# Optimization experiments

Hardware: AMD Instinct MI355X
Metric: run time of the kernel (lower is better)

Reference implementation:

```python
import jax, jax.numpy as jnp
import numpy as np

N_NODES = 100000
N_EDGES = 1600000
D_IN = 128
D_OUT = 128


def setup_inputs() -> dict:
    key = jax.random.key(0)
    k1, k2, k3, k4, k5 = jax.random.split(key, 5)
    x = jax.random.normal(k1, (N_NODES, D_IN), dtype=jnp.float32)
    row = jax.random.randint(k2, (N_EDGES,), 0, N_NODES, dtype=jnp.int32)
    col = jax.random.randint(k3, (N_EDGES,), 0, N_NODES, dtype=jnp.int32)
    edge_weight = jax.random.uniform(k4, (N_EDGES,), dtype=jnp.float32)
    stdv = 1.0 / np.sqrt(D_OUT)
    weight = jax.random.uniform(k5, (D_IN, D_OUT), dtype=jnp.float32,
                                minval=-stdv, maxval=stdv)
    return {"x": x, "row": row, "col": col,
            "edge_weight": edge_weight, "weight": weight}


def reference(x, row, col, edge_weight, weight):
    # support = x @ W  -- dense feature transform [N, D_OUT]
    support = jnp.matmul(x, weight)
    # out = adj @ support, adj sparse COO: out[row] += w * support[col]
    messages = edge_weight[:, None] * support[col]  # [E, D_OUT]
    out = jax.ops.segment_sum(messages, row, num_segments=N_NODES)
    return out
```

## Files before the change

### kernel.cpp

```cpp
#include <hip/hip_runtime.h>

#define N_NODES 100000
#define N_EDGES 1600000
#define D 128
#define D4 32

#define BM 128
#define GEMM_BLOCKS ((N_NODES + BM - 1) / BM)
#define LDK 136

typedef __attribute__((ext_vector_type(8))) short short8;
typedef __attribute__((ext_vector_type(4))) float floatx4;

__device__ __forceinline__ unsigned short f2bf(float f) {
    unsigned int b = __float_as_uint(f);
    b += 0x7FFFu + ((b >> 16) & 1u);
    return (unsigned short)(b >> 16);
}
__device__ __forceinline__ float bf2f(unsigned short u) {
    return __uint_as_float((unsigned int)u << 16);
}

__global__ __launch_bounds__(256) void w_prep(
    const float* __restrict__ W, unsigned short* __restrict__ wt)
{
    int idx = blockIdx.x * 256 + threadIdx.x;
    int k = idx >> 7, n = idx & 127;
    wt[(size_t)n * D + k] = f2bf(W[idx]);
}

__global__ __launch_bounds__(256, 4) void gemm_build(
    const float* __restrict__ x, const unsigned short* __restrict__ wt,
    unsigned short* __restrict__ sup,
    const int* __restrict__ row, const int* __restrict__ col,
    const float* __restrict__ ew,
    int* __restrict__ head, int4* __restrict__ entries)
{
    __shared__ unsigned short xs[BM * LDK];

    const int tid = threadIdx.x;
    const int brow = blockIdx.x * BM;

    {
        const float4* xv = reinterpret_cast<const float4*>(x);
        #pragma unroll
        for (int i = 0; i < 16; ++i) {
            int idx = tid + i * 256;
            int r = idx >> 5, k4 = idx & 31;
            int gr = brow + r;
            float4 v = (gr < N_NODES) ? xv[(size_t)gr * D4 + k4]
                                      : make_float4(0.f, 0.f, 0.f, 0.f);
            ushort4 p;
            p.x = f2bf(v.x); p.y = f2bf(v.y); p.z = f2bf(v.z); p.w = f2bf(v.w);
            *reinterpret_cast<ushort4*>(&xs[r * LDK + k4 * 4]) = p;
        }
    }
    __syncthreads();

    const int wave = tid >> 6;
    const int lane = tid & 63;
    const int l15  = lane & 15;
    const int lkg  = lane >> 4;
    const int lk8  = lkg * 8;

    floatx4 acc[2][8];
    #pragma unroll
    for (int m = 0; m < 2; ++m)
        #pragma unroll
        for (int n = 0; n < 8; ++n) acc[m][n] = (floatx4){0.f, 0.f, 0.f, 0.f};

    const short8* bv = reinterpret_cast<const short8*>(wt);
    const int wrow = wave * 32;
    #pragma unroll
    for (int kk = 0; kk < 4; ++kk) {
        int kb = kk * 32 + lk8;
        short8 a0 = *reinterpret_cast<const short8*>(&xs[(wrow + l15) * LDK + kb]);
        short8 a1 = *reinterpret_cast<const short8*>(&xs[(wrow + 16 + l15) * LDK + kb]);
        #pragma unroll
        for (int n = 0; n < 8; ++n) {
            short8 b = bv[(n * 16 + l15) * 16 + kk * 4 + lkg];
            acc[0][n] = __builtin_amdgcn_mfma_f32_16x16x32_bf16(a0, b, acc[0][n], 0, 0, 0);
            acc[1][n] = __builtin_amdgcn_mfma_f32_16x16x32_bf16(a1, b, acc[1][n], 0, 0, 0);
        }
    }

    const int rbase = brow + wrow + lkg * 4;
    #pragma unroll
    for (int m = 0; m < 2; ++m) {
        #pragma unroll
        for (int r = 0; r < 4; ++r) {
            int grow = rbase + m * 16 + r;
            if (grow < N_NODES) {
                #pragma unroll
                for (int n = 0; n < 8; ++n)
                    sup[(size_t)grow * D + n * 16 + l15] = f2bf(acc[m][n][r]);
            }
        }
    }

    for (int e = blockIdx.x * 256 + tid; e < N_EDGES; e += GEMM_BLOCKS * 256) {
        int nx = atomicExch(&head[row[e]], e);
        entries[e] = make_int4(nx, col[e], __float_as_int(ew[e]), 0);
    }
}

__global__ __launch_bounds__(256) void gather_list(
    const int* __restrict__ head, const int4* __restrict__ entries,
    const unsigned short* __restrict__ sup, float* __restrict__ out)
{
    const int half = threadIdx.x >> 5;
    const int lane = threadIdx.x & 31;
    const int node = blockIdx.x * 8 + half;

    float4 acc = {0.f, 0.f, 0.f, 0.f};

    int e = head[node];
    while (e >= 0) {
        int4 en = entries[e];
        float w = __int_as_float(en.z);
        ushort4 s = reinterpret_cast<const ushort4*>(sup + (size_t)en.y * D)[lane];
        acc.x = fmaf(w, bf2f(s.x), acc.x);
        acc.y = fmaf(w, bf2f(s.y), acc.y);
        acc.z = fmaf(w, bf2f(s.z), acc.z);
        acc.w = fmaf(w, bf2f(s.w), acc.w);
        e = en.x;
    }
    reinterpret_cast<float4*>(out)[(size_t)node * D4 + lane] = acc;
}

__device__ __forceinline__ void fma4(float4& a, float s, const float4& b) {
    a.x = fmaf(s, b.x, a.x);
    a.y = fmaf(s, b.y, a.y);
    a.z = fmaf(s, b.z, a.z);
    a.w = fmaf(s, b.w, a.w);
}

__global__ __launch_bounds__(256) void gemm_xw(
    const float* __restrict__ x, const float* __restrict__ W,
    unsigned short* __restrict__ sup)
{
    __shared__ float4 xs[32 * D4];
    const int tid = threadIdx.x;
    const int block_row = blockIdx.x * 32;

    const float4* xv = reinterpret_cast<const float4*>(x) + (size_t)block_row * D4;
    #pragma unroll
    for (int i = 0; i < 4; ++i) xs[tid + i * 256] = xv[tid + i * 256];
    __syncthreads();

    const int cg = tid & 31;
    const int rg = tid >> 5;
    const float4* Wv = reinterpret_cast<const float4*>(W);

    float4 acc0 = {0.f, 0.f, 0.f, 0.f};
    float4 acc1 = acc0, acc2 = acc0, acc3 = acc0;

    const int r0 = rg * 4;
    #pragma unroll 8
    for (int k4 = 0; k4 < D4; ++k4) {
        float4 xa = xs[(r0 + 0) * D4 + k4];
        float4 xb = xs[(r0 + 1) * D4 + k4];
        float4 xc = xs[(r0 + 2) * D4 + k4];
        float4 xd = xs[(r0 + 3) * D4 + k4];
        float4 w0 = Wv[(k4 * 4 + 0) * D4 + cg];
        fma4(acc0, xa.x, w0); fma4(acc1, xb.x, w0);
        fma4(acc2, xc.x, w0); fma4(acc3, xd.x, w0);
        float4 w1 = Wv[(k4 * 4 + 1) * D4 + cg];
        fma4(acc0, xa.y, w1); fma4(acc1, xb.y, w1);
        fma4(acc2, xc.y, w1); fma4(acc3, xd.y, w1);
        float4 w2 = Wv[(k4 * 4 + 2) * D4 + cg];
        fma4(acc0, xa.z, w2); fma4(acc1, xb.z, w2);
        fma4(acc2, xc.z, w2); fma4(acc3, xd.z, w2);
        float4 w3 = Wv[(k4 * 4 + 3) * D4 + cg];
        fma4(acc0, xa.w, w3); fma4(acc1, xb.w, w3);
        fma4(acc2, xc.w, w3); fma4(acc3, xd.w, w3);
    }

    ushort4 p;
    #define STORE_BF16(ACC, R)                                            \
        p.x = f2bf(ACC.x); p.y = f2bf(ACC.y);                             \
        p.z = f2bf(ACC.z); p.w = f2bf(ACC.w);                             \
        *reinterpret_cast<ushort4*>(sup + (size_t)(block_row + r0 + R) * D + cg * 4) = p;
    STORE_BF16(acc0, 0)
    STORE_BF16(acc1, 1)
    STORE_BF16(acc2, 2)
    STORE_BF16(acc3, 3)
    #undef STORE_BF16
}

__global__ __launch_bounds__(256) void scatter_edges(
    const int* __restrict__ row, const int* __restrict__ col,
    const float* __restrict__ ew, const unsigned short* __restrict__ sup,
    float* __restrict__ out)
{
    const int e = blockIdx.x * 8 + (threadIdx.x >> 5);
    if (e >= N_EDGES) return;
    const int lane = threadIdx.x & 31;

    const int r = row[e];
    const int c = col[e];
    const float w = ew[e];
    ushort4 s = reinterpret_cast<const ushort4*>(sup + (size_t)c * D)[lane];
    float* o = out + (size_t)r * D + lane * 4;
    atomicAdd(o + 0, w * bf2f(s.x));
    atomicAdd(o + 1, w * bf2f(s.y));
    atomicAdd(o + 2, w * bf2f(s.z));
    atomicAdd(o + 3, w * bf2f(s.w));
}

extern "C" void kernel_launch(void* const* d_in, const int* in_sizes, int n_in,
                              void* d_out, int out_size, void* d_ws, size_t ws_size,
                              hipStream_t stream)
{
    const float* x      = (const float*)d_in[0];
    const int*   row    = (const int*)d_in[1];
    const int*   col    = (const int*)d_in[2];
    const float* ew     = (const float*)d_in[3];
    const float* weight = (const float*)d_in[4];
    float* out = (float*)d_out;

    char* ws = (char*)d_ws;
    const size_t off_sup     = 0;
    const size_t off_head    = off_sup + (size_t)N_NODES * D * 2;
    const size_t off_entries = off_head + (((size_t)N_NODES * 4 + 15) & ~(size_t)15);
    const size_t off_wt      = off_entries + (size_t)N_EDGES * 16;
    const size_t required    = off_wt + (size_t)D * D * 2;

    unsigned short* sup = (unsigned short*)(ws + off_sup);

    if (ws_size >= required) {
        int*  head    = (int*)(ws + off_head);
        int4* entries = (int4*)(ws + off_entries);
        unsigned short* wt = (unsigned short*)(ws + off_wt);

        hipMemsetAsync(head, 0xFF, (size_t)N_NODES * 4, stream);
        w_prep<<<D * D / 256, 256, 0, stream>>>(weight, wt);

        gemm_build<<<GEMM_BLOCKS, 256, 0, stream>>>(
            x, wt, sup, row, col, ew, head, entries);

        gather_list<<<N_NODES / 8, 256, 0, stream>>>(head, entries, sup, out);
    } else {
        gemm_xw<<<N_NODES / 32, 256, 0, stream>>>(x, weight, sup);
        hipMemsetAsync(d_out, 0, (size_t)N_NODES * D * sizeof(float), stream);
        scatter_edges<<<N_EDGES / 8, 256, 0, stream>>>(row, col, ew, sup, out);
    }
}
```

Before: 213.6 us.

## Split list build into dedicated blocks and interleave four linked-list walks per warp

```diff
diff --git a/kernel.cpp b/kernel.cpp
--- a/kernel.cpp
+++ b/kernel.cpp
@@ -7,6 +7,8 @@
 
 #define BM 128
 #define GEMM_BLOCKS ((N_NODES + BM - 1) / BM)
+#define BUILD_BLOCKS 256
+#define TOTAL_BLOCKS (BUILD_BLOCKS + GEMM_BLOCKS)
 #define LDK 136
 
 typedef __attribute__((ext_vector_type(8))) short short8;
@@ -29,7 +31,7 @@
     wt[(size_t)n * D + k] = f2bf(W[idx]);
 }
 
-__global__ __launch_bounds__(256, 4) void gemm_build(
+__global__ __launch_bounds__(256, 4) void mega(
     const float* __restrict__ x, const unsigned short* __restrict__ wt,
     unsigned short* __restrict__ sup,
     const int* __restrict__ row, const int* __restrict__ col,
@@ -39,7 +41,16 @@
     __shared__ unsigned short xs[BM * LDK];
 
     const int tid = threadIdx.x;
-    const int brow = blockIdx.x * BM;
+
+    if (blockIdx.x < BUILD_BLOCKS) {
+        for (int e = blockIdx.x * 256 + tid; e < N_EDGES; e += BUILD_BLOCKS * 256) {
+            int nx = atomicExch(&head[row[e]], e);
+            entries[e] = make_int4(nx, col[e], __float_as_int(ew[e]), 0);
+        }
+        return;
+    }
+
+    const int brow = (blockIdx.x - BUILD_BLOCKS) * BM;
 
     {
         const float4* xv = reinterpret_cast<const float4*>(x);
@@ -61,7 +72,6 @@
     const int lane = tid & 63;
     const int l15  = lane & 15;
     const int lkg  = lane >> 4;
-    const int lk8  = lkg * 8;
 
     floatx4 acc[2][8];
     #pragma unroll
@@ -73,7 +83,7 @@
     const int wrow = wave * 32;
     #pragma unroll
     for (int kk = 0; kk < 4; ++kk) {
-        int kb = kk * 32 + lk8;
+        int kb = kk * 32 + lkg * 8;
         short8 a0 = *reinterpret_cast<const short8*>(&xs[(wrow + l15) * LDK + kb]);
         short8 a1 = *reinterpret_cast<const short8*>(&xs[(wrow + 16 + l15) * LDK + kb]);
         #pragma unroll
@@ -97,11 +107,6 @@
             }
         }
     }
-
-    for (int e = blockIdx.x * 256 + tid; e < N_EDGES; e += GEMM_BLOCKS * 256) {
-        int nx = atomicExch(&head[row[e]], e);
-        entries[e] = make_int4(nx, col[e], __float_as_int(ew[e]), 0);
-    }
 }
 
 __global__ __launch_bounds__(256) void gather_list(
@@ -110,22 +115,52 @@
 {
     const int half = threadIdx.x >> 5;
     const int lane = threadIdx.x & 31;
-    const int node = blockIdx.x * 8 + half;
-
-    float4 acc = {0.f, 0.f, 0.f, 0.f};
-
-    int e = head[node];
-    while (e >= 0) {
-        int4 en = entries[e];
-        float w = __int_as_float(en.z);
-        ushort4 s = reinterpret_cast<const ushort4*>(sup + (size_t)en.y * D)[lane];
-        acc.x = fmaf(w, bf2f(s.x), acc.x);
-        acc.y = fmaf(w, bf2f(s.y), acc.y);
-        acc.z = fmaf(w, bf2f(s.z), acc.z);
-        acc.w = fmaf(w, bf2f(s.w), acc.w);
-        e = en.x;
-    }
-    reinterpret_cast<float4*>(out)[(size_t)node * D4 + lane] = acc;
+    const int nb = blockIdx.x * 32 + half * 4;
+
+    float4 a0 = {0.f, 0.f, 0.f, 0.f};
+    float4 a1 = a0, a2 = a0, a3 = a0;
+
+    int e0 = head[nb + 0];
+    int e1 = head[nb + 1];
+    int e2 = head[nb + 2];
+    int e3 = head[nb + 3];
+
+    while (e0 >= 0 || e1 >= 0 || e2 >= 0 || e3 >= 0) {
+        int4 q0 = entries[e0 >= 0 ? e0 : 0];
+        int4 q1 = entries[e1 >= 0 ? e1 : 0];
+        int4 q2 = entries[e2 >= 0 ? e2 : 0];
+        int4 q3 = entries[e3 >= 0 ? e3 : 0];
+
+        ushort4 s0 = reinterpret_cast<const ushort4*>(sup + (size_t)q0.y * D)[lane];
+        ushort4 s1 = reinterpret_cast<const ushort4*>(sup + (size_t)q1.y * D)[lane];
+        ushort4 s2 = reinterpret_cast<const ushort4*>(sup + (size_t)q2.y * D)[lane];
+        ushort4 s3 = reinterpret_cast<const ushort4*>(sup + (size_t)q3.y * D)[lane];
+
+        float w0 = (e0 >= 0) ? __int_as_float(q0.z) : 0.f;
+        float w1 = (e1 >= 0) ? __int_as_float(q1.z) : 0.f;
+        float w2 = (e2 >= 0) ? __int_as_float(q2.z) : 0.f;
+        float w3 = (e3 >= 0) ? __int_as_float(q3.z) : 0.f;
+
+        a0.x = fmaf(w0, bf2f(s0.x), a0.x); a0.y = fmaf(w0, bf2f(s0.y), a0.y);
+        a0.z = fmaf(w0, bf2f(s0.z), a0.z); a0.w = fmaf(w0, bf2f(s0.w), a0.w);
+        a1.x = fmaf(w1, bf2f(s1.x), a1.x); a1.y = fmaf(w1, bf2f(s1.y), a1.y);
+        a1.z = fmaf(w1, bf2f(s1.z), a1.z); a1.w = fmaf(w1, bf2f(s1.w), a1.w);
+        a2.x = fmaf(w2, bf2f(s2.x), a2.x); a2.y = fmaf(w2, bf2f(s2.y), a2.y);
+        a2.z = fmaf(w2, bf2f(s2.z), a2.z); a2.w = fmaf(w2, bf2f(s2.w), a2.w);
+        a3.x = fmaf(w3, bf2f(s3.x), a3.x); a3.y = fmaf(w3, bf2f(s3.y), a3.y);
+        a3.z = fmaf(w3, bf2f(s3.z), a3.z); a3.w = fmaf(w3, bf2f(s3.w), a3.w);
+
+        e0 = (e0 >= 0) ? q0.x : -1;
+        e1 = (e1 >= 0) ? q1.x : -1;
+        e2 = (e2 >= 0) ? q2.x : -1;
+        e3 = (e3 >= 0) ? q3.x : -1;
+    }
+
+    float4* ov = reinterpret_cast<float4*>(out);
+    ov[(size_t)(nb + 0) * D4 + lane] = a0;
+    ov[(size_t)(nb + 1) * D4 + lane] = a1;
+    ov[(size_t)(nb + 2) * D4 + lane] = a2;
+    ov[(size_t)(nb + 3) * D4 + lane] = a3;
 }
 
 __device__ __forceinline__ void fma4(float4& a, float s, const float4& b) {
@@ -236,10 +271,10 @@
         hipMemsetAsync(head, 0xFF, (size_t)N_NODES * 4, stream);
         w_prep<<<D * D / 256, 256, 0, stream>>>(weight, wt);
 
-        gemm_build<<<GEMM_BLOCKS, 256, 0, stream>>>(
+        mega<<<TOTAL_BLOCKS, 256, 0, stream>>>(
             x, wt, sup, row, col, ew, head, entries);
 
-        gather_list<<<N_NODES / 8, 256, 0, stream>>>(head, entries, sup, out);
+        gather_list<<<N_NODES / 32, 256, 0, stream>>>(head, entries, sup, out);
     } else {
         gemm_xw<<<N_NODES / 32, 256, 0, stream>>>(x, weight, sup);
         hipMemsetAsync(d_out, 0, (size_t)N_NODES * D * sizeof(float), stream);
```

Result: faster. 184.2 us (-13.8%).

## Replace per-node linked lists with 32-node bucketed edge lists sorted in LDS

Applied to the files above, without the earlier changes.

```diff
diff --git a/kernel.cpp b/kernel.cpp
--- a/kernel.cpp
+++ b/kernel.cpp
@@ -7,7 +7,14 @@
 
 #define BM 128
 #define GEMM_BLOCKS ((N_NODES + BM - 1) / BM)
+#define FILL_BLOCKS 256
+#define TOTAL_BLOCKS (FILL_BLOCKS + GEMM_BLOCKS)
 #define LDK 136
+
+#define BK 32
+#define NBUCKETS (N_NODES / BK)
+#define CAPB 1024
+#define SPILL_CAP 32768
 
 typedef __attribute__((ext_vector_type(8))) short short8;
 typedef __attribute__((ext_vector_type(4))) float floatx4;
@@ -29,17 +36,36 @@
     wt[(size_t)n * D + k] = f2bf(W[idx]);
 }
 
-__global__ __launch_bounds__(256, 4) void gemm_build(
+__global__ __launch_bounds__(256, 4) void mega(
     const float* __restrict__ x, const unsigned short* __restrict__ wt,
     unsigned short* __restrict__ sup,
     const int* __restrict__ row, const int* __restrict__ col,
     const float* __restrict__ ew,
-    int* __restrict__ head, int4* __restrict__ entries)
+    int* __restrict__ len, int2* __restrict__ pairs,
+    int* __restrict__ spill_cnt, int4* __restrict__ spill)
 {
     __shared__ unsigned short xs[BM * LDK];
 
     const int tid = threadIdx.x;
-    const int brow = blockIdx.x * BM;
+
+    if (blockIdx.x < FILL_BLOCKS) {
+        for (int e = blockIdx.x * 256 + tid; e < N_EDGES; e += FILL_BLOCKS * 256) {
+            int r = row[e];
+            int b = r >> 5;
+            int packed = col[e] | ((r & 31) << 17);
+            int wb = __float_as_int(ew[e]);
+            int pos = atomicAdd(&len[b], 1);
+            if (pos < CAPB) {
+                pairs[(size_t)b * CAPB + pos] = make_int2(packed, wb);
+            } else {
+                int si = atomicAdd(spill_cnt, 1);
+                if (si < SPILL_CAP) spill[si] = make_int4(b, packed, wb, 0);
+            }
+        }
+        return;
+    }
+
+    const int brow = (blockIdx.x - FILL_BLOCKS) * BM;
 
     {
         const float4* xv = reinterpret_cast<const float4*>(x);
@@ -61,7 +87,6 @@
     const int lane = tid & 63;
     const int l15  = lane & 15;
     const int lkg  = lane >> 4;
-    const int lk8  = lkg * 8;
 
     floatx4 acc[2][8];
     #pragma unroll
@@ -73,7 +98,7 @@
     const int wrow = wave * 32;
     #pragma unroll
     for (int kk = 0; kk < 4; ++kk) {
-        int kb = kk * 32 + lk8;
+        int kb = kk * 32 + lkg * 8;
         short8 a0 = *reinterpret_cast<const short8*>(&xs[(wrow + l15) * LDK + kb]);
         short8 a1 = *reinterpret_cast<const short8*>(&xs[(wrow + 16 + l15) * LDK + kb]);
         #pragma unroll
@@ -97,35 +122,97 @@
             }
         }
     }
-
-    for (int e = blockIdx.x * 256 + tid; e < N_EDGES; e += GEMM_BLOCKS * 256) {
-        int nx = atomicExch(&head[row[e]], e);
-        entries[e] = make_int4(nx, col[e], __float_as_int(ew[e]), 0);
-    }
-}
-
-__global__ __launch_bounds__(256) void gather_list(
-    const int* __restrict__ head, const int4* __restrict__ entries,
+}
+
+__global__ __launch_bounds__(256) void gather_bucket(
+    const int* __restrict__ len, const int2* __restrict__ pairs,
+    const int* __restrict__ spill_cnt, const int4* __restrict__ spill,
     const unsigned short* __restrict__ sup, float* __restrict__ out)
 {
-    const int half = threadIdx.x >> 5;
-    const int lane = threadIdx.x & 31;
-    const int node = blockIdx.x * 8 + half;
-
-    float4 acc = {0.f, 0.f, 0.f, 0.f};
-
-    int e = head[node];
-    while (e >= 0) {
-        int4 en = entries[e];
-        float w = __int_as_float(en.z);
-        ushort4 s = reinterpret_cast<const ushort4*>(sup + (size_t)en.y * D)[lane];
-        acc.x = fmaf(w, bf2f(s.x), acc.x);
-        acc.y = fmaf(w, bf2f(s.y), acc.y);
-        acc.z = fmaf(w, bf2f(s.z), acc.z);
-        acc.w = fmaf(w, bf2f(s.w), acc.w);
-        e = en.x;
-    }
-    reinterpret_cast<float4*>(out)[(size_t)node * D4 + lane] = acc;
+    __shared__ int2 sorted[CAPB];
+    __shared__ int bins[BK];
+    __shared__ int boffs[BK + 1];
+    __shared__ int bcur[BK];
+
+    const int b = blockIdx.x;
+    const int tid = threadIdx.x;
+    const int cnt = len[b];
+    const int cl = cnt < CAPB ? cnt : CAPB;
+    const int2* pp = pairs + (size_t)b * CAPB;
+
+    if (tid < BK) bins[tid] = 0;
+    __syncthreads();
+
+    for (int i = tid; i < cl; i += 256)
+        atomicAdd(&bins[pp[i].x >> 17], 1);
+    __syncthreads();
+
+    if (tid == 0) {
+        int s = 0;
+        #pragma unroll
+        for (int j = 0; j < BK; ++j) { boffs[j] = s; bcur[j] = s; s += bins[j]; }
+        boffs[BK] = s;
+    }
+    __syncthreads();
+
+    for (int i = tid; i < cl; i += 256) {
+        int2 p = pp[i];
+        int pos = atomicAdd(&bcur[p.x >> 17], 1);
+        sorted[pos] = p;
+    }
+    __syncthreads();
+
+    const int half = tid >> 5;
+    const int lane = tid & 31;
+    const int sc = *spill_cnt;
+    const ushort4* supv = reinterpret_cast<const ushort4*>(sup);
+    float4* ov = reinterpret_cast<float4*>(out);
+
+    #pragma unroll
+    for (int j = 0; j < 4; ++j) {
+        const int loc = half * 4 + j;
+        const int s0 = boffs[loc], s1 = boffs[loc + 1];
+        float4 a = {0.f, 0.f, 0.f, 0.f};
+
+        int k = s0;
+        for (; k + 4 <= s1; k += 4) {
+            int2 p0 = sorted[k], p1 = sorted[k + 1];
+            int2 p2 = sorted[k + 2], p3 = sorted[k + 3];
+            ushort4 q0 = supv[(size_t)(p0.x & 0x1FFFF) * D4 + lane];
+            ushort4 q1 = supv[(size_t)(p1.x & 0x1FFFF) * D4 + lane];
+            ushort4 q2 = supv[(size_t)(p2.x & 0x1FFFF) * D4 + lane];
+            ushort4 q3 = supv[(size_t)(p3.x & 0x1FFFF) * D4 + lane];
+            float w0 = __int_as_float(p0.y), w1 = __int_as_float(p1.y);
+            float w2 = __int_as_float(p2.y), w3 = __int_as_float(p3.y);
+            a.x = fmaf(w0, bf2f(q0.x), a.x); a.y = fmaf(w0, bf2f(q0.y), a.y);
+            a.z = fmaf(w0, bf2f(q0.z), a.z); a.w = fmaf(w0, bf2f(q0.w), a.w);
+            a.x = fmaf(w1, bf2f(q1.x), a.x); a.y = fmaf(w1, bf2f(q1.y), a.y);
+            a.z = fmaf(w1, bf2f(q1.z), a.z); a.w = fmaf(w1, bf2f(q1.w), a.w);
+            a.x = fmaf(w2, bf2f(q2.x), a.x); a.y = fmaf(w2, bf2f(q2.y), a.y);
+            a.z = fmaf(w2, bf2f(q2.z), a.z); a.w = fmaf(w2, bf2f(q2.w), a.w);
+            a.x = fmaf(w3, bf2f(q3.x), a.x); a.y = fmaf(w3, bf2f(q3.y), a.y);
+            a.z = fmaf(w3, bf2f(q3.z), a.z); a.w = fmaf(w3, bf2f(q3.w), a.w);
+        }
+        for (; k < s1; ++k) {
+            int2 p = sorted[k];
+            ushort4 q = supv[(size_t)(p.x & 0x1FFFF) * D4 + lane];
+            float w = __int_as_float(p.y);
+            a.x = fmaf(w, bf2f(q.x), a.x); a.y = fmaf(w, bf2f(q.y), a.y);
+            a.z = fmaf(w, bf2f(q.z), a.z); a.w = fmaf(w, bf2f(q.w), a.w);
+        }
+
+        for (int i2 = 0; i2 < sc; ++i2) {
+            int4 sp = spill[i2];
+            if (sp.x == b && (sp.y >> 17) == loc) {
+                ushort4 q = supv[(size_t)(sp.y & 0x1FFFF) * D4 + lane];
+                float w = __int_as_float(sp.z);
+                a.x = fmaf(w, bf2f(q.x), a.x); a.y = fmaf(w, bf2f(q.y), a.y);
+                a.z = fmaf(w, bf2f(q.z), a.z); a.w = fmaf(w, bf2f(q.w), a.w);
+            }
+        }
+
+        ov[(size_t)(b * BK + loc) * D4 + lane] = a;
+    }
 }
 
 __device__ __forceinline__ void fma4(float4& a, float s, const float4& b) {
@@ -220,26 +307,32 @@
     float* out = (float*)d_out;
 
     char* ws = (char*)d_ws;
-    const size_t off_sup     = 0;
-    const size_t off_head    = off_sup + (size_t)N_NODES * D * 2;
-    const size_t off_entries = off_head + (((size_t)N_NODES * 4 + 15) & ~(size_t)15);
-    const size_t off_wt      = off_entries + (size_t)N_EDGES * 16;
-    const size_t required    = off_wt + (size_t)D * D * 2;
+    const size_t off_sup    = 0;
+    const size_t off_pairs  = off_sup + (size_t)N_NODES * D * 2;
+    const size_t off_len    = off_pairs + (size_t)NBUCKETS * CAPB * 8;
+    const size_t off_wt     = off_len + (size_t)NBUCKETS * 4;
+    const size_t off_scnt   = off_wt + (size_t)D * D * 2;
+    const size_t off_spill  = off_scnt + 16;
+    const size_t required   = off_spill + (size_t)SPILL_CAP * 16;
 
     unsigned short* sup = (unsigned short*)(ws + off_sup);
 
     if (ws_size >= required) {
-        int*  head    = (int*)(ws + off_head);
-        int4* entries = (int4*)(ws + off_entries);
+        int2* pairs = (int2*)(ws + off_pairs);
+        int*  len   = (int*)(ws + off_len);
         unsigned short* wt = (unsigned short*)(ws + off_wt);
-
-        hipMemsetAsync(head, 0xFF, (size_t)N_NODES * 4, stream);
+        int*  scnt  = (int*)(ws + off_scnt);
+        int4* spill = (int4*)(ws + off_spill);
+
+        hipMemsetAsync(len, 0, (size_t)NBUCKETS * 4, stream);
+        hipMemsetAsync(scnt, 0, 16, stream);
         w_prep<<<D * D / 256, 256, 0, stream>>>(weight, wt);
 
-        gemm_build<<<GEMM_BLOCKS, 256, 0, stream>>>(
-            x, wt, sup, row, col, ew, head, entries);
-
-        gather_list<<<N_NODES / 8, 256, 0, stream>>>(head, entries, sup, out);
+        mega<<<TOTAL_BLOCKS, 256, 0, stream>>>(
+            x, wt, sup, row, col, ew, len, pairs, scnt, spill);
+
+        gather_bucket<<<NBUCKETS, 256, 0, stream>>>(
+            len, pairs, scnt, spill, sup, out);
     } else {
         gemm_xw<<<N_NODES / 32, 256, 0, stream>>>(x, weight, sup);
         hipMemsetAsync(d_out, 0, (size_t)N_NODES * D * sizeof(float), stream);
```

Measured after the change: 252.2 us. +18.1%, slower.
